# Optimization experiments

Measured on AMD Instinct MI355X. Metric: run time of the kernel, lower is better.

## Reference

```python
import jax, jax.numpy as jnp
import numpy as np

HIDDEN = 2048
NUM_V = 16
NUM_K = 8
HK = 128
HV = 128
KCONV = 4
KEY_DIM = NUM_K * HK      # 1024
VALUE_DIM = NUM_V * HV    # 2048
CONV_DIM = 2 * KEY_DIM + VALUE_DIM  # 4096
R = NUM_V // NUM_K        # 2
L2_EPS = 1e-6
NORM_EPS = 1e-6


def setup_inputs() -> dict:
    key = jax.random.key(0)
    ks = jax.random.split(key, 8)
    s = 0.02
    return {
        "hidden_states": jax.random.normal(ks[0], (1, 1024, HIDDEN), jnp.float32),
        "w_qkvz": jax.random.normal(ks[1], (2 * KEY_DIM + 2 * VALUE_DIM, HIDDEN), jnp.float32) * s,
        "w_ba": jax.random.normal(ks[2], (2 * NUM_V, HIDDEN), jnp.float32) * s,
        "conv_w": jax.random.normal(ks[3], (CONV_DIM, KCONV), jnp.float32) * s,
        "dt_bias": jnp.ones((NUM_V,), jnp.float32),
        "A_log": jnp.log(jax.random.uniform(ks[4], (NUM_V,), jnp.float32, 1e-3, 16.0)),
        "norm_weight": jnp.ones((HV,), jnp.float32),
        "w_out": jax.random.normal(ks[5], (HIDDEN, VALUE_DIM), jnp.float32) * s,
    }


def reference(hidden_states, w_qkvz, w_ba, conv_w, dt_bias, A_log, norm_weight, w_out):
    B, T, _ = hidden_states.shape
    # --- input projections ---
    qkvz = hidden_states @ w_qkvz.T                     # [B,T,2K+2V]
    ba = hidden_states @ w_ba.T                         # [B,T,2*Hv]
    # fix_query_key_value_ordering: group by k-head, layout [hk, hk, r*hv, r*hv]
    qkvz = qkvz.reshape(B, T, NUM_K, 2 * HK + 2 * R * HV)
    q, k, v, z = jnp.split(qkvz, [HK, 2 * HK, 2 * HK + R * HV], axis=3)
    v = v.reshape(B, T, NUM_V, HV)
    z = z.reshape(B, T, NUM_V, HV)
    ba = ba.reshape(B, T, NUM_K, 2 * R)
    b = ba[..., :R].reshape(B, T, NUM_V)
    a = ba[..., R:].reshape(B, T, NUM_V)
    # --- depthwise causal conv1d + silu over concatenated q,k,v ---
    mixed = jnp.concatenate(
        [q.reshape(B, T, KEY_DIM), k.reshape(B, T, KEY_DIM), v.reshape(B, T, VALUE_DIM)], axis=-1
    )
    xc = mixed.transpose(0, 2, 1)                       # [B,C,T]
    yc = jax.lax.conv_general_dilated(
        xc, conv_w[:, None, :], (1,), [(KCONV - 1, 0)],
        feature_group_count=CONV_DIM, dimension_numbers=("NCH", "OIH", "NCH"),
    )
    yc = jax.nn.silu(yc).transpose(0, 2, 1)             # [B,T,C]
    q, k, v = jnp.split(yc, [KEY_DIM, 2 * KEY_DIM], axis=-1)
    q = q.reshape(B, T, NUM_K, HK)
    k = k.reshape(B, T, NUM_K, HK)
    v = v.reshape(B, T, NUM_V, HV)
    # --- gates ---
    beta = jax.nn.sigmoid(b)                            # [B,T,Hv]
    g = -jnp.exp(A_log) * jax.nn.softplus(a + dt_bias)  # [B,T,Hv] (log decay, <=0)
    # GQA expansion of q,k to value heads
    q = jnp.repeat(q, R, axis=2)                        # [B,T,Hv,hk]
    k = jnp.repeat(k, R, axis=2)
    # l2 norm on q,k (use_qk_l2norm_in_kernel=True)
    q = q * jax.lax.rsqrt(jnp.sum(q * q, -1, keepdims=True) + L2_EPS)
    k = k * jax.lax.rsqrt(jnp.sum(k * k, -1, keepdims=True) + L2_EPS)
    scale = HK ** -0.5
    # --- gated delta rule recurrence ---
    def step(S, xs):
        qt, kt, vt, gt, bt = xs                          # per-timestep slices
        S = S * jnp.exp(gt)[..., None, None]             # decay state [B,Hv,hk,hv]
        kv = jnp.einsum("bhk,bhkv->bhv", kt, S)          # readout at k_t
        delta = (vt - kv) * bt[..., None]                # beta-gated delta
        S = S + jnp.einsum("bhk,bhv->bhkv", kt, delta)
        o = jnp.einsum("bhk,bhkv->bhv", qt * scale, S)
        return S, o

    S0 = jnp.zeros((B, NUM_V, HK, HV), hidden_states.dtype)
    xs = (
        q.transpose(1, 0, 2, 3), k.transpose(1, 0, 2, 3), v.transpose(1, 0, 2, 3),
        g.transpose(1, 0, 2), beta.transpose(1, 0, 2),
    )
    _, o = jax.lax.scan(step, S0, xs)                   # o: [T,B,Hv,hv]
    o = o.transpose(1, 0, 2, 3)                         # [B,T,Hv,hv]
    # --- gated RMSNorm (gate applied before normalization, Mamba2/Qwen3Next style) ---
    xf = o.astype(jnp.float32) * jax.nn.silu(z.astype(jnp.float32))
    var = jnp.mean(xf * xf, -1, keepdims=True)
    xn = xf * jax.lax.rsqrt(var + NORM_EPS) * norm_weight
    # --- output projection ---
    return xn.reshape(B, T, VALUE_DIM) @ w_out.T
```

## Files before the change

### kernel.cpp

```cpp
#include <hip/hip_runtime.h>
#include <math.h>

#define T_LEN   1024
#define HIDDEN  2048
#define QKVZ_N  6144
#define VAL_DIM 2048

typedef _Float16 half8 __attribute__((ext_vector_type(8)));
typedef _Float16 half4 __attribute__((ext_vector_type(4)));
typedef _Float16 half2t __attribute__((ext_vector_type(2)));
typedef float floatx4 __attribute__((ext_vector_type(4)));

__device__ __forceinline__ float sigmoidf_(float x) { return 1.f / (1.f + expf(-x)); }

__global__ __launch_bounds__(256) void cvt_h(const float* __restrict__ src,
                                             _Float16* __restrict__ dst, int n4) {
    const int i = blockIdx.x * 256 + threadIdx.x;
    if (i < n4) {
        const float4 v = ((const float4*)src)[i];
        half4 h;
        h[0] = (_Float16)v.x; h[1] = (_Float16)v.y;
        h[2] = (_Float16)v.z; h[3] = (_Float16)v.w;
        *(half4*)&dst[i * 4] = h;
    }
}

template <typename OutT>
__global__ __launch_bounds__(256) void gemm_h16(const _Float16* __restrict__ A,
                                                const _Float16* __restrict__ W,
                                                OutT* __restrict__ C,
                                                int MB, int NB, int K) {
    const int N = NB * 128;
    const int l = blockIdx.x;
    const int x = l & 7;
    const int tt = l >> 3;
    const int mb = tt % MB;
    const int nb = x + 8 * (tt / MB);
    const int m0 = mb * 128, n0 = nb * 128;

    const int t = threadIdx.x;
    const int kq = t & 3;
    const int r0 = t >> 2;
    const int wave = t >> 6;
    const int lane = t & 63;
    const int wr = (wave >> 1) * 64;
    const int wc = (wave & 1) * 64;
    const int l15 = lane & 15;
    const int quad = lane >> 4;

    __shared__ __align__(16) _Float16 Ah[4096];
    __shared__ __align__(16) _Float16 Bh[4096];

    floatx4 acc[4][4];
#pragma unroll
    for (int i = 0; i < 4; ++i)
#pragma unroll
        for (int j = 0; j < 4; ++j) acc[i][j] = 0;

    for (int k0 = 0; k0 < K; k0 += 32) {
        half8 ag[2], bg[2];
#pragma unroll
        for (int p = 0; p < 2; ++p) {
            const int r = r0 + p * 64;
            ag[p] = *(const half8*)(A + (size_t)(m0 + r) * K + k0 + kq * 8);
            bg[p] = *(const half8*)(W + (size_t)(n0 + r) * K + k0 + kq * 8);
        }
        __syncthreads();
#pragma unroll
        for (int p = 0; p < 2; ++p) {
            const int r = r0 + p * 64;
            const int chunk = r * 4 + (kq ^ (r & 3));
            *(half8*)&Ah[chunk * 8] = ag[p];
            *(half8*)&Bh[chunk * 8] = bg[p];
        }
        __syncthreads();
        half8 af[4], bf[4];
#pragma unroll
        for (int mt = 0; mt < 4; ++mt) {
            const int m = wr + mt * 16 + l15;
            af[mt] = *(const half8*)&Ah[(m * 4 + (quad ^ (m & 3))) * 8];
        }
#pragma unroll
        for (int nt = 0; nt < 4; ++nt) {
            const int n = wc + nt * 16 + l15;
            bf[nt] = *(const half8*)&Bh[(n * 4 + (quad ^ (n & 3))) * 8];
        }
#pragma unroll
        for (int mt = 0; mt < 4; ++mt)
#pragma unroll
            for (int nt = 0; nt < 4; ++nt)
                acc[mt][nt] = __builtin_amdgcn_mfma_f32_16x16x32_f16(
                    af[mt], bf[nt], acc[mt][nt], 0, 0, 0);
    }
#pragma unroll
    for (int mt = 0; mt < 4; ++mt)
#pragma unroll
        for (int nt = 0; nt < 4; ++nt) {
            const int c = n0 + wc + nt * 16 + l15;
#pragma unroll
            for (int reg = 0; reg < 4; ++reg) {
                const int r = m0 + wr + mt * 16 + quad * 4 + reg;
                C[(size_t)r * N + c] = (OutT)acc[mt][nt][reg];
            }
        }
}

__global__ __launch_bounds__(256) void gemm_ba(const float* __restrict__ A,
                                               const float* __restrict__ W,
                                               float* __restrict__ C) {
    const int m = blockIdx.x;
    const int tid = threadIdx.x;
    const int kl = tid & 31;
    const int ng = tid >> 5;
    const float* Arow = A + (size_t)m * 2048;

    float4 a4[16];
#pragma unroll
    for (int j = 0; j < 16; ++j)
        a4[j] = *(const float4*)(Arow + j * 128 + kl * 4);

#pragma unroll
    for (int nn = 0; nn < 4; ++nn) {
        const int n = nn * 8 + ng;
        const float* Wrow = W + (size_t)n * 2048;
        float acc = 0.f;
#pragma unroll
        for (int j = 0; j < 16; ++j) {
            const float4 w4 = *(const float4*)(Wrow + j * 128 + kl * 4);
            acc = fmaf(a4[j].x, w4.x, acc);
            acc = fmaf(a4[j].y, w4.y, acc);
            acc = fmaf(a4[j].z, w4.z, acc);
            acc = fmaf(a4[j].w, w4.w, acc);
        }
        acc += __shfl_xor(acc, 1, 64);
        acc += __shfl_xor(acc, 2, 64);
        acc += __shfl_xor(acc, 4, 64);
        acc += __shfl_xor(acc, 8, 64);
        acc += __shfl_xor(acc, 16, 64);
        if (kl == 0) C[m * 32 + n] = acc;
    }
}

__global__ __launch_bounds__(256) void conv_silu(const _Float16* __restrict__ qkvz,
                                                 const float* __restrict__ conv_w,
                                                 _Float16* __restrict__ qc,
                                                 _Float16* __restrict__ kc,
                                                 _Float16* __restrict__ vc) {
    const int idx = blockIdx.x * 256 + threadIdx.x;
    const int t = idx >> 12;
    const int c = idx & 4095;
    int col;
    _Float16* dst;
    if (c < 1024) {
        col = ((c >> 7) * 768) + (c & 127);
        dst = qc + t * 1024 + c;
    } else if (c < 2048) {
        const int cc = c - 1024;
        col = ((cc >> 7) * 768) + 128 + (cc & 127);
        dst = kc + t * 1024 + cc;
    } else {
        const int cc = c - 2048;
        col = ((cc >> 8) * 768) + 256 + (cc & 255);
        dst = vc + t * 2048 + cc;
    }
    const float w0 = conv_w[c * 4 + 0];
    const float w1 = conv_w[c * 4 + 1];
    const float w2 = conv_w[c * 4 + 2];
    const float w3 = conv_w[c * 4 + 3];
    float acc = (float)qkvz[(size_t)t * QKVZ_N + col] * w3;
    if (t >= 1) acc = fmaf((float)qkvz[(size_t)(t - 1) * QKVZ_N + col], w2, acc);
    if (t >= 2) acc = fmaf((float)qkvz[(size_t)(t - 2) * QKVZ_N + col], w1, acc);
    if (t >= 3) acc = fmaf((float)qkvz[(size_t)(t - 3) * QKVZ_N + col], w0, acc);
    *dst = (_Float16)(acc * sigmoidf_(acc));
}

__global__ __launch_bounds__(64) void l2norm_qk(_Float16* __restrict__ qc,
                                                _Float16* __restrict__ kc) {
    const int b = blockIdx.x;
    const int t = b >> 4;
    const int hh = b & 15;
    _Float16* p;
    float extra;
    if (hh < 8) { p = qc + t * 1024 + hh * 128; extra = 0.08838834764831845f; }
    else        { p = kc + t * 1024 + (hh - 8) * 128; extra = 1.f; }
    const int j = threadIdx.x * 2;
    half2t x = *(const half2t*)(p + j);
    const float x0 = (float)x[0], x1 = (float)x[1];
    float ss = x0 * x0 + x1 * x1;
#pragma unroll
    for (int m = 1; m < 64; m <<= 1) ss += __shfl_xor(ss, m, 64);
    const float r = rsqrtf(ss + 1e-6f) * extra;
    half2t y; y[0] = (_Float16)(x0 * r); y[1] = (_Float16)(x1 * r);
    *(half2t*)(p + j) = y;
}

__global__ __launch_bounds__(256) void gates(const float* __restrict__ ba,
                                             const float* __restrict__ dt_bias,
                                             const float* __restrict__ A_log,
                                             float* __restrict__ lgd,
                                             float* __restrict__ bet) {
    const int i = blockIdx.x * 256 + threadIdx.x;
    const int t = i >> 4;
    const int vh = i & 15;
    const int kh = vh >> 1;
    const int r = vh & 1;
    const float b = ba[t * 32 + kh * 4 + r];
    const float a = ba[t * 32 + kh * 4 + 2 + r];
    bet[i] = 1.f / (1.f + expf(-b));
    const float x = a + dt_bias[vh];
    const float sp = (x > 0.f) ? (x + log1pf(expf(-x))) : log1pf(expf(x));
    lgd[i] = -expf(A_log[vh]) * sp;
}

__global__ __launch_bounds__(256) void chunk_prep(
    const _Float16* __restrict__ qch, const _Float16* __restrict__ kch,
    const _Float16* __restrict__ vch, const float* __restrict__ lgd,
    const float* __restrict__ bet, _Float16* __restrict__ CH,
    float* __restrict__ gamC) {
    const int blk = blockIdx.x;
    const int c = blk >> 4, h = blk & 15, kh = h >> 1;
    const int c0 = c * 64;
    const int tid = threadIdx.x, lane = tid & 63, wave = tid >> 6;
    const int l15 = lane & 15, quad = lane >> 4;

    __shared__ __align__(16) _Float16 Ksh[8192];
    __shared__ __align__(16) _Float16 Qsh[8192];
    __shared__ float Amat[64 * 65];
    __shared__ float Gs[64], Bets[64], Gam[64];

    {
        const int t = tid >> 2, kc0 = (tid & 3) * 4;
        const size_t gb = (size_t)(c0 + t) * 1024 + kh * 128;
#pragma unroll
        for (int i = 0; i < 4; ++i) {
            const int kc = kc0 + i;
            half8 kv = *(const half8*)(kch + gb + kc * 8);
            half8 qv = *(const half8*)(qch + gb + kc * 8);
            const int chl = t * 16 + (kc ^ (t & 15));
            *(half8*)&Ksh[chl * 8] = kv;
            *(half8*)&Qsh[chl * 8] = qv;
        }
    }
    if (tid < 64) {
        float g = lgd[(size_t)(c0 + tid) * 16 + h];
#pragma unroll
        for (int off = 1; off < 64; off <<= 1) {
            float y = __shfl_up(g, off, 64);
            if (tid >= off) g += y;
        }
        Gs[tid] = g;
        Gam[tid] = expf(g);
        Bets[tid] = bet[(size_t)(c0 + tid) * 16 + h];
    }
    __syncthreads();

    _Float16* CHb = CH + (size_t)(c * 16 + h) * 36864;
    _Float16* Ug = CHb;
    _Float16* Wtg = CHb + 8192;
    _Float16* Khg = CHb + 16384;
    _Float16* Qgg = CHb + 24576;
    _Float16* Lg = CHb + 32768;

    {
        floatx4 accKK[4], accQK[4];
#pragma unroll
        for (int tt = 0; tt < 4; ++tt) { accKK[tt] = 0; accQK[tt] = 0; }
        half8 bfK[4];
#pragma unroll
        for (int ks = 0; ks < 4; ++ks) {
            const int i = wave * 16 + l15;
            const int kc = ks * 4 + quad;
            bfK[ks] = *(const half8*)&Ksh[(i * 16 + (kc ^ (i & 15))) * 8];
        }
#pragma unroll
        for (int tt = 0; tt < 4; ++tt) {
            const int t = tt * 16 + l15;
#pragma unroll
            for (int ks = 0; ks < 4; ++ks) {
                const int kc = ks * 4 + quad;
                const int chl = (t * 16 + (kc ^ (t & 15))) * 8;
                half8 afK = *(const half8*)&Ksh[chl];
                half8 afQ = *(const half8*)&Qsh[chl];
                accKK[tt] = __builtin_amdgcn_mfma_f32_16x16x32_f16(afK, bfK[ks], accKK[tt], 0, 0, 0);
                accQK[tt] = __builtin_amdgcn_mfma_f32_16x16x32_f16(afQ, bfK[ks], accQK[tt], 0, 0, 0);
            }
        }
        const int ii = wave * 16 + l15;
        const float Gi = Gs[ii];
#pragma unroll
        for (int tt = 0; tt < 4; ++tt)
#pragma unroll
            for (int r = 0; r < 4; ++r) {
                const int t = tt * 16 + quad * 4 + r;
                const float Gt = Gs[t];
                const float ratio = (ii <= t) ? expf(Gt - Gi) : 0.f;
                if (ii < t) Amat[t * 65 + ii] = Bets[t] * ratio * accKK[tt][r];
                Lg[t * 64 + ii] = (_Float16)((ii <= t) ? ratio * accQK[tt][r] : 0.f);
            }
    }
    __syncthreads();

    {
        const int j = tid;
        float x[64];
        if (j < 128) {
#pragma unroll
            for (int t = 0; t < 64; ++t)
                x[t] = Bets[t] * (float)vch[(size_t)(c0 + t) * 2048 + h * 128 + j];
        } else {
            const int k = j - 128;
#pragma unroll
            for (int t = 0; t < 64; ++t) {
                const int chl = t * 16 + ((k >> 3) ^ (t & 15));
                x[t] = Bets[t] * Gam[t] * (float)Ksh[chl * 8 + (k & 7)];
            }
        }
#pragma unroll
        for (int t = 1; t < 64; ++t) {
            float acc = 0.f;
#pragma unroll
            for (int i = 0; i < t; ++i) acc = fmaf(Amat[t * 65 + i], x[i], acc);
            x[t] -= acc;
        }
        if (j < 128) {
#pragma unroll
            for (int t = 0; t < 64; t += 4) {
                half4 w4;
                w4[0] = (_Float16)x[t]; w4[1] = (_Float16)x[t + 1];
                w4[2] = (_Float16)x[t + 2]; w4[3] = (_Float16)x[t + 3];
                *(half4*)&Wtg[j * 64 + t] = w4;
            }
        } else {
            const int k = j - 128;
#pragma unroll
            for (int t = 0; t < 64; ++t) Ug[t * 128 + k] = (_Float16)x[t];
        }
    }

    {
        const float g63 = Gs[63];
        const int k = tid >> 1, cb = (tid & 1) * 32;
#pragma unroll
        for (int cc = 0; cc < 32; cc += 4) {
            half4 o4;
#pragma unroll
            for (int u = 0; u < 4; ++u) {
                const int ci = cb + cc + u;
                const int chl = ci * 16 + ((k >> 3) ^ (ci & 15));
                o4[u] = (_Float16)(expf(g63 - Gs[ci]) * (float)Ksh[chl * 8 + (k & 7)]);
            }
            *(half4*)&Khg[k * 64 + cb + cc] = o4;
        }
        const int cq = tid >> 2, kb = (tid & 3) * 4;
        const float gam = Gam[cq];
#pragma unroll
        for (int kc = 0; kc < 4; ++kc) {
            const int kcc = kb + kc;
            half8 q8 = *(const half8*)&Qsh[(cq * 16 + (kcc ^ (cq & 15))) * 8];
            half8 s8;
#pragma unroll
            for (int u = 0; u < 8; ++u) s8[u] = (_Float16)(gam * (float)q8[u]);
            *(half8*)&Qgg[cq * 128 + kcc * 8] = s8;
        }
        if (tid == 0) gamC[c * 16 + h] = Gam[63];
    }
}

__global__ __launch_bounds__(256) void chunk_scan(const _Float16* __restrict__ CH,
                                                  const float* __restrict__ gamC,
                                                  float* __restrict__ o) {
    const int h = blockIdx.x >> 1, vs = blockIdx.x & 1;
    const int tid = threadIdx.x, lane = tid & 63, wave = tid >> 6;
    const int l15 = lane & 15, quad = lane >> 4;
    const int vrow = wave * 16 + l15;

    __shared__ __align__(16) _Float16 Sh[8192];
    __shared__ __align__(16) _Float16 Dt[4096];
    __shared__ __align__(16) _Float16 LUg[8704];
    __shared__ __align__(16) _Float16 LWt[4608];
    __shared__ __align__(16) _Float16 LKh[9216];
    __shared__ __align__(16) _Float16 LQg[8704];
    __shared__ __align__(16) _Float16 LLg[4608];

    floatx4 Sacc[8];
#pragma unroll
    for (int kt = 0; kt < 8; ++kt) Sacc[kt] = 0;
    for (int i = tid; i < 1024; i += 256) *(int4*)&Sh[i * 8] = make_int4(0, 0, 0, 0);
    __syncthreads();

    for (int c = 0; c < 16; ++c) {
        const _Float16* CHb = CH + (size_t)(c * 16 + h) * 36864;
        {
            const int4* src = (const int4*)CHb;
#pragma unroll
            for (int i = 0; i < 4; ++i) {
                const int idx = tid + i * 256;
                *(int4*)&LUg[((idx >> 4) * 17 + (idx & 15)) * 8] = src[idx];
            }
        }
        {
            const int4* src = (const int4*)(CHb + 8192 + vs * 4096);
#pragma unroll
            for (int i = 0; i < 2; ++i) {
                const int idx = tid + i * 256;
                *(int4*)&LWt[((idx >> 3) * 9 + (idx & 7)) * 8] = src[idx];
            }
        }
        {
            const int4* src = (const int4*)(CHb + 16384);
#pragma unroll
            for (int i = 0; i < 4; ++i) {
                const int idx = tid + i * 256;
                *(int4*)&LKh[((idx >> 3) * 9 + (idx & 7)) * 8] = src[idx];
            }
        }
        {
            const int4* src = (const int4*)(CHb + 24576);
#pragma unroll
            for (int i = 0; i < 4; ++i) {
                const int idx = tid + i * 256;
                *(int4*)&LQg[((idx >> 4) * 17 + (idx & 15)) * 8] = src[idx];
            }
        }
        {
            const int4* src = (const int4*)(CHb + 32768);
#pragma unroll
            for (int i = 0; i < 2; ++i) {
                const int idx = tid + i * 256;
                *(int4*)&LLg[((idx >> 3) * 9 + (idx & 7)) * 8] = src[idx];
            }
        }
        __syncthreads();

        half8 bs[4];
#pragma unroll
        for (int ks = 0; ks < 4; ++ks) {
            const int kc = ks * 4 + quad;
            bs[ks] = *(const half8*)&Sh[(vrow * 16 + (kc ^ (vrow & 15))) * 8];
        }
#pragma unroll
        for (int ct = 0; ct < 4; ++ct) {
            floatx4 xa = {0.f, 0.f, 0.f, 0.f};
#pragma unroll
            for (int ks = 0; ks < 4; ++ks) {
                half8 af = *(const half8*)&LUg[((ct * 16 + l15) * 17 + ks * 4 + quad) * 8];
                xa = __builtin_amdgcn_mfma_f32_16x16x32_f16(af, bs[ks], xa, 0, 0, 0);
            }
            half4 w4 = *(const half4*)&LWt[(vrow * 9 + ct * 2 + (quad >> 1)) * 8 + (quad & 1) * 4];
            half4 d4;
#pragma unroll
            for (int r = 0; r < 4; ++r) d4[r] = (_Float16)((float)w4[r] - xa[r]);
            const int cc = ct * 2 + (quad >> 1);
            *(half4*)&Dt[(vrow * 8 + (cc ^ (vrow & 7))) * 8 + (quad & 1) * 4] = d4;
        }
        half8 bd[2];
#pragma unroll
        for (int cs = 0; cs < 2; ++cs) {
            const int cc = cs * 4 + quad;
            bd[cs] = *(const half8*)&Dt[(vrow * 8 + (cc ^ (vrow & 7))) * 8];
        }
#pragma unroll
        for (int ct = 0; ct < 4; ++ct) {
            floatx4 oa = {0.f, 0.f, 0.f, 0.f};
#pragma unroll
            for (int ks = 0; ks < 4; ++ks) {
                half8 af = *(const half8*)&LQg[((ct * 16 + l15) * 17 + ks * 4 + quad) * 8];
                oa = __builtin_amdgcn_mfma_f32_16x16x32_f16(af, bs[ks], oa, 0, 0, 0);
            }
#pragma unroll
            for (int cs = 0; cs < 2; ++cs) {
                half8 af = *(const half8*)&LLg[((ct * 16 + l15) * 9 + cs * 4 + quad) * 8];
                oa = __builtin_amdgcn_mfma_f32_16x16x32_f16(af, bd[cs], oa, 0, 0, 0);
            }
            const int tg = c * 64 + ct * 16 + quad * 4;
            const int col = h * 128 + vs * 64 + vrow;
#pragma unroll
            for (int r = 0; r < 4; ++r) o[(size_t)(tg + r) * 2048 + col] = oa[r];
        }
        const float gC = gamC[c * 16 + h];
#pragma unroll
        for (int kt = 0; kt < 8; ++kt) {
#pragma unroll
            for (int r = 0; r < 4; ++r) Sacc[kt][r] *= gC;
#pragma unroll
            for (int cs = 0; cs < 2; ++cs) {
                half8 af = *(const half8*)&LKh[((kt * 16 + l15) * 9 + cs * 4 + quad) * 8];
                Sacc[kt] = __builtin_amdgcn_mfma_f32_16x16x32_f16(af, bd[cs], Sacc[kt], 0, 0, 0);
            }
        }
#pragma unroll
        for (int kt = 0; kt < 8; ++kt) {
            const int kc = kt * 2 + (quad >> 1);
            half4 s4;
#pragma unroll
            for (int r = 0; r < 4; ++r) s4[r] = (_Float16)Sacc[kt][r];
            *(half4*)&Sh[(vrow * 16 + (kc ^ (vrow & 15))) * 8 + (quad & 1) * 4] = s4;
        }
        __syncthreads();
    }
}

__global__ __launch_bounds__(64) void gated_norm(const float* __restrict__ o,
                                                 const _Float16* __restrict__ qkvz,
                                                 const float* __restrict__ nw,
                                                 _Float16* __restrict__ xn) {
    const int b = blockIdx.x;
    const int t = b >> 4;
    const int vh = b & 15;
    const int kh = vh >> 1;
    const int r = vh & 1;
    const float* op = o + (size_t)t * 2048 + vh * 128;
    const _Float16* zp = qkvz + (size_t)t * QKVZ_N + kh * 768 + 512 + r * 128;
    const int j = threadIdx.x * 2;
    const float2 ov = *(const float2*)(op + j);
    const half2t zv = *(const half2t*)(zp + j);
    const float z0 = (float)zv[0], z1 = (float)zv[1];
    const float f0 = ov.x * z0 / (1.f + expf(-z0));
    const float f1 = ov.y * z1 / (1.f + expf(-z1));
    float ss = f0 * f0 + f1 * f1;
#pragma unroll
    for (int m = 1; m < 64; m <<= 1) ss += __shfl_xor(ss, m, 64);
    const float rs = rsqrtf(ss * (1.f / 128.f) + 1e-6f);
    _Float16* xp = xn + (size_t)t * 2048 + vh * 128;
    half2t y;
    y[0] = (_Float16)(f0 * rs * nw[j]);
    y[1] = (_Float16)(f1 * rs * nw[j + 1]);
    *(half2t*)(xp + j) = y;
}

extern "C" void kernel_launch(void* const* d_in, const int* in_sizes, int n_in,
                              void* d_out, int out_size, void* d_ws, size_t ws_size,
                              hipStream_t stream) {
    const float* hidden  = (const float*)d_in[0];
    const float* w_qkvz  = (const float*)d_in[1];
    const float* w_ba    = (const float*)d_in[2];
    const float* conv_w  = (const float*)d_in[3];
    const float* dt_bias = (const float*)d_in[4];
    const float* A_log   = (const float*)d_in[5];
    const float* norm_w  = (const float*)d_in[6];
    const float* w_out   = (const float*)d_in[7];
    float* out = (float*)d_out;

    char* w = (char*)d_ws;
    _Float16*  qkvz_h = (_Float16*)(w);
    float*     ba     = (float*)(w + 12582912);
    _Float16*  qch    = (_Float16*)(w + 12713984);
    _Float16*  kch    = (_Float16*)(w + 14811136);
    _Float16*  vch    = (_Float16*)(w + 16908288);
    float*     lgd    = (float*)(w + 21102592);
    float*     bet    = (float*)(w + 21168128);
    float*     gamC   = (float*)(w + 21233664);
    float*     o      = (float*)(w + 21237760);
    _Float16*  hid_h  = (_Float16*)(w + 21237760);
    _Float16*  wqk_h  = (_Float16*)(w + 29626368);
    _Float16*  CH     = (_Float16*)(w + 29626368);
    _Float16*  xn_h   = (_Float16*)(w + 29626368 + 18874368);
    _Float16*  wout_h = (_Float16*)(w + 54792192);

    cvt_h<<<(HIDDEN * T_LEN / 4 + 255) / 256, 256, 0, stream>>>(hidden, hid_h,
                                                                HIDDEN * T_LEN / 4);
    cvt_h<<<(QKVZ_N * HIDDEN / 4 + 255) / 256, 256, 0, stream>>>(w_qkvz, wqk_h,
                                                                 QKVZ_N * HIDDEN / 4);
    cvt_h<<<(VAL_DIM * HIDDEN / 4 + 255) / 256, 256, 0, stream>>>(w_out, wout_h,
                                                                  VAL_DIM * HIDDEN / 4);

    gemm_h16<_Float16><<<8 * 48, 256, 0, stream>>>(hid_h, wqk_h, qkvz_h, 8, 48, HIDDEN);
    gemm_ba<<<T_LEN, 256, 0, stream>>>(hidden, w_ba, ba);
    conv_silu<<<(T_LEN * 4096) / 256, 256, 0, stream>>>(qkvz_h, conv_w, qch, kch, vch);
    l2norm_qk<<<T_LEN * 16, 64, 0, stream>>>(qch, kch);
    gates<<<(T_LEN * 16) / 256, 256, 0, stream>>>(ba, dt_bias, A_log, lgd, bet);
    chunk_prep<<<256, 256, 0, stream>>>(qch, kch, vch, lgd, bet, CH, gamC);
    chunk_scan<<<32, 256, 0, stream>>>(CH, gamC, o);
    gated_norm<<<T_LEN * 16, 64, 0, stream>>>(o, qkvz_h, norm_w, xn_h);
    gemm_h16<float><<<8 * 16, 256, 0, stream>>>(xn_h, wout_h, out, 8, 16, HIDDEN);
}
```

Before: 333.9 us.

## Merge conversions, fuse gates into ba GEMM, use direct global-to-LDS loads

Three fp32-to-fp16 conversion launches are merged into a single launch, and the gates computation is folded into the ba projection kernel so the intermediate ba buffer and one launch go away. The fp16 GEMM now loads tiles straight from global memory into LDS with global_load_lds, keeping the XOR swizzle and removing the register staging. It also sets launch_bounds min-blocks to 2. The direct-to-LDS path changes the write pattern and drops the overlap of global loads with the previous barrier, which could hurt load latency hiding.

```diff
diff --git a/kernel.cpp b/kernel.cpp
--- a/kernel.cpp
+++ b/kernel.cpp
@@ -13,23 +13,34 @@
 
 __device__ __forceinline__ float sigmoidf_(float x) { return 1.f / (1.f + expf(-x)); }
 
-__global__ __launch_bounds__(256) void cvt_h(const float* __restrict__ src,
-                                             _Float16* __restrict__ dst, int n4) {
-    const int i = blockIdx.x * 256 + threadIdx.x;
-    if (i < n4) {
-        const float4 v = ((const float4*)src)[i];
-        half4 h;
-        h[0] = (_Float16)v.x; h[1] = (_Float16)v.y;
-        h[2] = (_Float16)v.z; h[3] = (_Float16)v.w;
-        *(half4*)&dst[i * 4] = h;
-    }
+__device__ __forceinline__ void gl_lds16(const _Float16* g, _Float16* l) {
+    __builtin_amdgcn_global_load_lds(
+        (const __attribute__((address_space(1))) void*)g,
+        (__attribute__((address_space(3))) void*)l, 16, 0, 0);
+}
+
+__global__ __launch_bounds__(256) void cvt3(const float* __restrict__ s0, _Float16* __restrict__ d0, int n0,
+                                            const float* __restrict__ s1, _Float16* __restrict__ d1, int n1,
+                                            const float* __restrict__ s2, _Float16* __restrict__ d2, int n2) {
+    int i = blockIdx.x * 256 + threadIdx.x;
+    const float* s;
+    _Float16* d;
+    if (i < n0) { s = s0; d = d0; }
+    else if (i < n0 + n1) { s = s1; d = d1; i -= n0; }
+    else if (i < n0 + n1 + n2) { s = s2; d = d2; i -= n0 + n1; }
+    else return;
+    const float4 v = ((const float4*)s)[i];
+    half4 h;
+    h[0] = (_Float16)v.x; h[1] = (_Float16)v.y;
+    h[2] = (_Float16)v.z; h[3] = (_Float16)v.w;
+    *(half4*)&d[i * 4] = h;
 }
 
 template <typename OutT>
-__global__ __launch_bounds__(256) void gemm_h16(const _Float16* __restrict__ A,
-                                                const _Float16* __restrict__ W,
-                                                OutT* __restrict__ C,
-                                                int MB, int NB, int K) {
+__global__ __launch_bounds__(256, 2) void gemm_h16(const _Float16* __restrict__ A,
+                                                   const _Float16* __restrict__ W,
+                                                   OutT* __restrict__ C,
+                                                   int MB, int NB, int K) {
     const int N = NB * 128;
     const int l = blockIdx.x;
     const int x = l & 7;
@@ -39,8 +50,6 @@
     const int m0 = mb * 128, n0 = nb * 128;
 
     const int t = threadIdx.x;
-    const int kq = t & 3;
-    const int r0 = t >> 2;
     const int wave = t >> 6;
     const int lane = t & 63;
     const int wr = (wave >> 1) * 64;
@@ -51,6 +60,9 @@
     __shared__ __align__(16) _Float16 Ah[4096];
     __shared__ __align__(16) _Float16 Bh[4096];
 
+    const int sr = lane >> 2;
+    const int skq = lane & 3;
+
     floatx4 acc[4][4];
 #pragma unroll
     for (int i = 0; i < 4; ++i)
@@ -58,20 +70,14 @@
         for (int j = 0; j < 4; ++j) acc[i][j] = 0;
 
     for (int k0 = 0; k0 < K; k0 += 32) {
-        half8 ag[2], bg[2];
+        __syncthreads();
 #pragma unroll
         for (int p = 0; p < 2; ++p) {
-            const int r = r0 + p * 64;
-            ag[p] = *(const half8*)(A + (size_t)(m0 + r) * K + k0 + kq * 8);
-            bg[p] = *(const half8*)(W + (size_t)(n0 + r) * K + k0 + kq * 8);
-        }
-        __syncthreads();
-#pragma unroll
-        for (int p = 0; p < 2; ++p) {
-            const int r = r0 + p * 64;
-            const int chunk = r * 4 + (kq ^ (r & 3));
-            *(half8*)&Ah[chunk * 8] = ag[p];
-            *(half8*)&Bh[chunk * 8] = bg[p];
+            const int r = p * 64 + wave * 16 + sr;
+            const int kc = skq ^ (r & 3);
+            const int lbase = (p * 256 + wave * 64) * 8;
+            gl_lds16(A + (size_t)(m0 + r) * K + k0 + kc * 8, &Ah[lbase]);
+            gl_lds16(W + (size_t)(n0 + r) * K + k0 + kc * 8, &Bh[lbase]);
         }
         __syncthreads();
         half8 af[4], bf[4];
@@ -105,14 +111,18 @@
         }
 }
 
-__global__ __launch_bounds__(256) void gemm_ba(const float* __restrict__ A,
-                                               const float* __restrict__ W,
-                                               float* __restrict__ C) {
+__global__ __launch_bounds__(256) void gemm_ba_gates(const float* __restrict__ A,
+                                                     const float* __restrict__ W,
+                                                     const float* __restrict__ dt_bias,
+                                                     const float* __restrict__ A_log,
+                                                     float* __restrict__ lgd,
+                                                     float* __restrict__ bet) {
     const int m = blockIdx.x;
     const int tid = threadIdx.x;
     const int kl = tid & 31;
     const int ng = tid >> 5;
     const float* Arow = A + (size_t)m * 2048;
+    __shared__ float sba[32];
 
     float4 a4[16];
 #pragma unroll
@@ -137,7 +147,17 @@
         acc += __shfl_xor(acc, 4, 64);
         acc += __shfl_xor(acc, 8, 64);
         acc += __shfl_xor(acc, 16, 64);
-        if (kl == 0) C[m * 32 + n] = acc;
+        if (kl == 0) sba[n] = acc;
+    }
+    __syncthreads();
+    if (tid < 16) {
+        const int vh = tid, kh = vh >> 1, r = vh & 1;
+        const float b = sba[kh * 4 + r];
+        const float a = sba[kh * 4 + 2 + r];
+        bet[m * 16 + vh] = 1.f / (1.f + expf(-b));
+        const float xx = a + dt_bias[vh];
+        const float sp = (xx > 0.f) ? (xx + log1pf(expf(-xx))) : log1pf(expf(xx));
+        lgd[m * 16 + vh] = -expf(A_log[vh]) * sp;
     }
 }
 
@@ -194,24 +214,6 @@
     *(half2t*)(p + j) = y;
 }
 
-__global__ __launch_bounds__(256) void gates(const float* __restrict__ ba,
-                                             const float* __restrict__ dt_bias,
-                                             const float* __restrict__ A_log,
-                                             float* __restrict__ lgd,
-                                             float* __restrict__ bet) {
-    const int i = blockIdx.x * 256 + threadIdx.x;
-    const int t = i >> 4;
-    const int vh = i & 15;
-    const int kh = vh >> 1;
-    const int r = vh & 1;
-    const float b = ba[t * 32 + kh * 4 + r];
-    const float a = ba[t * 32 + kh * 4 + 2 + r];
-    bet[i] = 1.f / (1.f + expf(-b));
-    const float x = a + dt_bias[vh];
-    const float sp = (x > 0.f) ? (x + log1pf(expf(-x))) : log1pf(expf(x));
-    lgd[i] = -expf(A_log[vh]) * sp;
-}
-
 __global__ __launch_bounds__(256) void chunk_prep(
     const _Float16* __restrict__ qch, const _Float16* __restrict__ kch,
     const _Float16* __restrict__ vch, const float* __restrict__ lgd,
@@ -543,7 +545,6 @@
 
     char* w = (char*)d_ws;
     _Float16*  qkvz_h = (_Float16*)(w);
-    float*     ba     = (float*)(w + 12582912);
     _Float16*  qch    = (_Float16*)(w + 12713984);
     _Float16*  kch    = (_Float16*)(w + 14811136);
     _Float16*  vch    = (_Float16*)(w + 16908288);
@@ -557,18 +558,17 @@
     _Float16*  xn_h   = (_Float16*)(w + 29626368 + 18874368);
     _Float16*  wout_h = (_Float16*)(w + 54792192);
 
-    cvt_h<<<(HIDDEN * T_LEN / 4 + 255) / 256, 256, 0, stream>>>(hidden, hid_h,
-                                                                HIDDEN * T_LEN / 4);
-    cvt_h<<<(QKVZ_N * HIDDEN / 4 + 255) / 256, 256, 0, stream>>>(w_qkvz, wqk_h,
-                                                                 QKVZ_N * HIDDEN / 4);
-    cvt_h<<<(VAL_DIM * HIDDEN / 4 + 255) / 256, 256, 0, stream>>>(w_out, wout_h,
-                                                                  VAL_DIM * HIDDEN / 4);
+    const int n0 = HIDDEN * T_LEN / 4;
+    const int n1 = QKVZ_N * HIDDEN / 4;
+    const int n2 = VAL_DIM * HIDDEN / 4;
+    cvt3<<<(n0 + n1 + n2 + 255) / 256, 256, 0, stream>>>(hidden, hid_h, n0,
+                                                         w_qkvz, wqk_h, n1,
+                                                         w_out, wout_h, n2);
 
     gemm_h16<_Float16><<<8 * 48, 256, 0, stream>>>(hid_h, wqk_h, qkvz_h, 8, 48, HIDDEN);
-    gemm_ba<<<T_LEN, 256, 0, stream>>>(hidden, w_ba, ba);
+    gemm_ba_gates<<<T_LEN, 256, 0, stream>>>(hidden, w_ba, dt_bias, A_log, lgd, bet);
     conv_silu<<<(T_LEN * 4096) / 256, 256, 0, stream>>>(qkvz_h, conv_w, qch, kch, vch);
     l2norm_qk<<<T_LEN * 16, 64, 0, stream>>>(qch, kch);
-    gates<<<(T_LEN * 16) / 256, 256, 0, stream>>>(ba, dt_bias, A_log, lgd, bet);
     chunk_prep<<<256, 256, 0, stream>>>(qch, kch, vch, lgd, bet, CH, gamC);
     chunk_scan<<<32, 256, 0, stream>>>(CH, gamC, o);
     gated_norm<<<T_LEN * 16, 64, 0, stream>>>(o, qkvz_h, norm_w, xn_h);
```

Result: faster. 316.7 us (-5.1%).
